# Kernel optimization log

Hardware: AMD Instinct MI355X
Metric: run time of the kernel (lower is better)

The kernel has to match this reference:

```python
import jax, jax.numpy as jnp
import numpy as np
from jax import lax

B, T, H, L = 64, 512, 768, 32
PAD = 0  # label_pad_token_id (NER_PAD_ID)


def setup_inputs() -> dict:
    key = jax.random.key(0)
    ks = jax.random.split(key, 8)
    hidden_states = jax.random.normal(ks[0], (B, T, H), jnp.float32)
    lengths = jax.random.randint(ks[1], (B,), T // 2, T + 1)
    attention_mask = (jnp.arange(T)[None, :] < lengths[:, None]).astype(jnp.int32)
    labels = jax.random.randint(ks[2], (B, T), 0, L).astype(jnp.int32)
    W = jax.random.normal(ks[3], (H, L), jnp.float32) * 0.02
    b = jnp.zeros((L,), jnp.float32)
    start_transitions = jax.random.uniform(ks[4], (L,), jnp.float32, -0.1, 0.1)
    end_transitions = jax.random.uniform(ks[5], (L,), jnp.float32, -0.1, 0.1)
    transitions = jax.random.uniform(ks[6], (L, L), jnp.float32, -0.1, 0.1)
    return dict(hidden_states=hidden_states, attention_mask=attention_mask,
                labels=labels, W=W, b=b, start_transitions=start_transitions,
                end_transitions=end_transitions, transitions=transitions)


def reference(hidden_states, attention_mask, labels, W, b,
              start_transitions, end_transitions, transitions):
    mask = attention_mask.astype(bool)          # [B,T], mask[:,0] all True
    mf = attention_mask.astype(hidden_states.dtype)
    # Dropout is identity at inference; emissions = Linear(hidden)
    emissions = hidden_states @ W + b            # [B,T,L]
    lengths = mask.sum(axis=1)                   # [B]

    # ---- CRF numerator (score of gold path) ----
    em_sc = jnp.take_along_axis(emissions, labels[..., None].astype(jnp.int32), axis=2)[..., 0]  # [B,T]
    tr_sc = transitions[labels[:, :-1], labels[:, 1:]]                                           # [B,T-1]
    last_tags = jnp.take_along_axis(labels, (lengths - 1)[:, None], axis=1)[:, 0]
    numer = (start_transitions[labels[:, 0]] + em_sc[:, 0]
             + jnp.sum((em_sc[:, 1:] + tr_sc) * mf[:, 1:], axis=1)
             + end_transitions[last_tags])

    # ---- CRF partition function (forward algorithm, scan over time) ----
    score0 = start_transitions + emissions[:, 0]                 # [B,L]
    em_rest = emissions[:, 1:].swapaxes(0, 1)                    # [T-1,B,L]
    m_rest = mask[:, 1:].T                                       # [T-1,B]

    def fstep(score, inp):
        em_t, m_t = inp
        nxt = jax.nn.logsumexp(score[:, :, None] + transitions[None], axis=1) + em_t
        return jnp.where(m_t[:, None], nxt, score), None

    scoreT, _ = lax.scan(fstep, score0, (em_rest, m_rest))
    denom = jax.nn.logsumexp(scoreT + end_transitions, axis=1)
    loss = -jnp.sum(numer - denom)               # torchcrf reduction='sum', times -1

    # ---- Viterbi decode ----
    def vstep(score, inp):
        em_t, m_t = inp
        x = score[:, :, None] + transitions[None]  # [B,L(prev),L(cur)]
        idx = jnp.argmax(x, axis=1)                # best prev tag per cur tag
        nxt = jnp.max(x, axis=1) + em_t
        return jnp.where(m_t[:, None], nxt, score), idx

    vT, hist = lax.scan(vstep, score0, (em_rest, m_rest))  # hist: [T-1,B,L]
    best_last = jnp.argmax(vT + end_transitions, axis=1).astype(jnp.int32)  # [B]
    last_idx = (lengths - 1).astype(jnp.int32)

    def bstep(carry, inp):
        h_t, t = inp                                            # h_t: [B,L]
        prev = jnp.take_along_axis(h_t, carry[:, None], axis=1)[:, 0].astype(jnp.int32)
        new_carry = jnp.where(t < last_idx, prev, best_last)
        out = jnp.where(t == last_idx, best_last,
                        jnp.where(t > last_idx, PAD, prev))
        return new_carry, out

    ts = jnp.arange(T - 2, -1, -1)
    _, outs = lax.scan(bstep, best_last, (hist[::-1], ts))      # outs: [T-1,B] for t=T-2..0
    tag_last = jnp.where(last_idx == T - 1, best_last, PAD)
    pred_labels = jnp.concatenate([jnp.flip(outs, 0), tag_last[None]], axis=0).T  # [B,T]
    return loss, pred_labels
```

## Files before the change

### kernel.cpp

```cpp
#include <hip/hip_runtime.h>

constexpr int Bn = 64, Tn = 512, Hn = 768, Ln = 32;

__global__ __launch_bounds__(256) void emis_gemm(const float* __restrict__ hs,
                                                 const float* __restrict__ W,
                                                 const float* __restrict__ bias,
                                                 float* __restrict__ em) {
  __shared__ __align__(16) float4 wl[Hn * 8];
  __shared__ __align__(16) float4 cbuf[128 * 8];
  const int tid = threadIdx.x;
  for (int it = tid; it < Hn * 8; it += 256) wl[it] = ((const float4*)W)[it];
  __syncthreads();
  const int half = tid >> 7;
  const int r = tid & 127;
  const long row = (long)blockIdx.x * 128 + r;
  const float* hb = hs + row * Hn + half * 384;
  const float4* wp = wl + half * 384 * 8;
  float4 acc[8];
#pragma unroll
  for (int c = 0; c < 8; ++c) acc[c] = make_float4(0.f, 0.f, 0.f, 0.f);
  for (int k4 = 0; k4 < 384; k4 += 4) {
    float4 h = *(const float4*)(hb + k4);
#pragma unroll
    for (int kk = 0; kk < 4; ++kk) {
      float hv = kk == 0 ? h.x : kk == 1 ? h.y : kk == 2 ? h.z : h.w;
      const float4* wr = wp + (k4 + kk) * 8;
#pragma unroll
      for (int c = 0; c < 8; ++c) {
        float4 wv = wr[c];
        acc[c].x = fmaf(hv, wv.x, acc[c].x);
        acc[c].y = fmaf(hv, wv.y, acc[c].y);
        acc[c].z = fmaf(hv, wv.z, acc[c].z);
        acc[c].w = fmaf(hv, wv.w, acc[c].w);
      }
    }
  }
  if (half == 1) {
#pragma unroll
    for (int c = 0; c < 8; ++c) cbuf[r * 8 + c] = acc[c];
  }
  __syncthreads();
  if (half == 0) {
#pragma unroll
    for (int c = 0; c < 8; ++c) {
      float4 p = cbuf[r * 8 + c];
      float4 bv = ((const float4*)bias)[c];
      float4 o = make_float4(acc[c].x + p.x + bv.x, acc[c].y + p.y + bv.y,
                             acc[c].z + p.z + bv.z, acc[c].w + p.w + bv.w);
      *(float4*)(em + row * Ln + c * 4) = o;
    }
  }
}

__global__ __launch_bounds__(512) void crf_scan(const float* __restrict__ em,
                                                const int* __restrict__ mask,
                                                const int* __restrict__ labels,
                                                const float* __restrict__ startT,
                                                const float* __restrict__ endT,
                                                const float* __restrict__ trans,
                                                float* __restrict__ outp) {
  __shared__ unsigned char hist[8][Tn][Ln];
  __shared__ __align__(16) float stage[8][64];
  __shared__ unsigned char Ctab[8][32][32];
  __shared__ int bnd[8][33];
  __shared__ int bl_lds[8];
  __shared__ int len_lds[8];

  const int tid = threadIdx.x;
  const int wid = tid >> 6;
  const int lane = tid & 63;
  const int half = lane >> 5;
  const int j = lane & 31;
  const bool is_vit = wid < 4;
  const int wb = ((wid & 3) << 1) + half;
  const int batch = blockIdx.x * 8 + wb;

  int s = 0;
  for (int t = j; t < Tn; t += 32) s += mask[batch * Tn + t];
#pragma unroll
  for (int m = 1; m <= 16; m <<= 1) s += __shfl_xor(s, m);
  const int len = s;
  const int lw = max(len, __shfl_xor(len, 32));
  const float* emb = em + (long)batch * Tn * Ln;

  if (is_vit) {
    if (j == 0) len_lds[wb] = len;
    float tr[32];
#pragma unroll
    for (int i = 0; i < 32; ++i) tr[i] = trans[i * Ln + j];
    float score = startT[j] + emb[j];
    float emn = emb[Ln + j];
    for (int t = 1; t < lw; ++t) {
      float em_t = emn;
      int tn = t + 1 < Tn ? t + 1 : Tn - 1;
      emn = emb[tn * Ln + j];
      stage[wid][lane] = score;
      const float* sb = &stage[wid][half * 32];
      float v[32];
#pragma unroll
      for (int q4 = 0; q4 < 8; ++q4) {
        float4 s4 = *(const float4*)(sb + q4 * 4);
        v[q4 * 4 + 0] = s4.x + tr[q4 * 4 + 0];
        v[q4 * 4 + 1] = s4.y + tr[q4 * 4 + 1];
        v[q4 * 4 + 2] = s4.z + tr[q4 * 4 + 2];
        v[q4 * 4 + 3] = s4.w + tr[q4 * 4 + 3];
      }
      float w[16];
#pragma unroll
      for (int q = 0; q < 16; ++q) w[q] = fmaxf(v[q], v[q + 16]);
#pragma unroll
      for (int sz = 8; sz >= 1; sz >>= 1)
#pragma unroll
        for (int q = 0; q < sz; ++q) w[q] = fmaxf(w[q], w[q + sz]);
      const float mv = w[0];
      int mi = 31;
#pragma unroll
      for (int i = 31; i >= 0; --i) mi = (v[i] == mv) ? i : mi;
      hist[wb][t - 1][j] = (unsigned char)mi;
      score = (t < len) ? (mv + em_t) : score;
    }
    for (int x = j; x < (Tn + 1 - len) * Ln; x += 32) {
      int rr = len - 1 + (x >> 5);
      hist[wb][rr][x & 31] = (unsigned char)(x & 31);
    }
    float bv = score + endT[j];
    int bj = j;
#pragma unroll
    for (int m = 1; m <= 16; m <<= 1) {
      float ov = __shfl_xor(bv, m);
      int oi = __shfl_xor(bj, m);
      if (ov > bv || (ov == bv && oi < bj)) { bv = ov; bj = oi; }
    }
    if (j == 0) bl_lds[wb] = bj;
  } else {
    float et[32];
#pragma unroll
    for (int i = 0; i < 32; ++i) et[i] = __expf(trans[i * Ln + j]);
    float score = startT[j] + emb[j];
    float emn = emb[Ln + j];
    for (int t = 1; t < lw; ++t) {
      float em_t = emn;
      int tn = t + 1 < Tn ? t + 1 : Tn - 1;
      emn = emb[tn * Ln + j];
      float s0 = __shfl(score, lane & 32);
      float e = __expf(score - s0);
      stage[wid][lane] = e;
      const float* eb = &stage[wid][half * 32];
      float a0 = 0.f, a1 = 0.f, a2 = 0.f, a3 = 0.f;
#pragma unroll
      for (int q = 0; q < 8; ++q) {
        float4 ev = *(const float4*)(eb + q * 4);
        a0 = fmaf(ev.x, et[q * 4 + 0], a0);
        a1 = fmaf(ev.y, et[q * 4 + 1], a1);
        a2 = fmaf(ev.z, et[q * 4 + 2], a2);
        a3 = fmaf(ev.w, et[q * 4 + 3], a3);
      }
      float nx = s0 + __logf((a0 + a1) + (a2 + a3)) + em_t;
      score = (t < len) ? nx : score;
    }
    float v = score + endT[j];
    float mx = v;
#pragma unroll
    for (int m = 1; m <= 16; m <<= 1) mx = fmaxf(mx, __shfl_xor(mx, m));
    float ssum = __expf(v - mx);
#pragma unroll
    for (int m = 1; m <= 16; m <<= 1) ssum += __shfl_xor(ssum, m);
    float denom = mx + __logf(ssum);
    float part = 0.f;
    const int* lab = labels + batch * Tn;
    for (int t = j; t < Tn; t += 32) {
      int lt = lab[t];
      if (t == 0)
        part += startT[lt] + emb[lt];
      else if (t < len)
        part += emb[t * Ln + lt] + trans[lab[t - 1] * Ln + lt];
    }
#pragma unroll
    for (int m = 1; m <= 16; m <<= 1) part += __shfl_xor(part, m);
    if (j == 0) {
      int lastl = lab[len - 1];
      atomicAdd(outp, denom - (part + endT[lastl]));
    }
  }
  __syncthreads();

  {
    const int wb2 = wid;
    const int batch2 = blockIdx.x * 8 + wb2;
    const int len2 = len_lds[wb2];
    const int best_last = bl_lds[wb2];
    const int kh2 = lane >> 5;
    int F[16];
#pragma unroll
    for (int kk = 0; kk < 16; ++kk) F[kk] = hist[wb2][16 * (kh2 * 16 + kk) + 15][j];
    for (int s2 = 14; s2 >= 0; --s2) {
#pragma unroll
      for (int kk = 0; kk < 16; ++kk) F[kk] = hist[wb2][16 * (kh2 * 16 + kk) + s2][F[kk]];
    }
#pragma unroll
    for (int kk = 0; kk < 16; ++kk) Ctab[wb2][kh2 * 16 + kk][j] = (unsigned char)F[kk];
    __syncthreads();
    if (lane == 0) {
      int c = best_last;
      bnd[wb2][32] = c;
      for (int k = 31; k >= 0; --k) {
        c = Ctab[wb2][k][c];
        bnd[wb2][k] = c;
      }
    }
    __syncthreads();
    if (lane < 32) {
      int c = bnd[wb2][lane + 1];
      float* po = outp + 1 + (long)batch2 * Tn;
#pragma unroll
      for (int s3 = 15; s3 >= 0; --s3) {
        int t = 16 * lane + s3;
        c = hist[wb2][t][c];
        po[t] = (t < len2) ? (float)c : 0.0f;
      }
    }
  }
}

extern "C" void kernel_launch(void* const* d_in, const int* in_sizes, int n_in,
                              void* d_out, int out_size, void* d_ws, size_t ws_size,
                              hipStream_t stream) {
  const float* hs = (const float*)d_in[0];
  const int* mask = (const int*)d_in[1];
  const int* labels = (const int*)d_in[2];
  const float* W = (const float*)d_in[3];
  const float* b = (const float*)d_in[4];
  const float* startT = (const float*)d_in[5];
  const float* endT = (const float*)d_in[6];
  const float* trans = (const float*)d_in[7];
  float* out = (float*)d_out;
  float* em = (float*)d_ws;

  emis_gemm<<<256, 256, 0, stream>>>(hs, W, b, em);
  hipMemsetAsync(d_out, 0, sizeof(float), stream);
  crf_scan<<<8, 512, 0, stream>>>(em, mask, labels, startT, endT, trans, out);
}
```

Measured before the change: 406.1 us.

## Spread CRF scan across more blocks and stage hidden rows via LDS in GEMM

The CRF scan now runs 32 blocks of 128 threads, each handling 2 batch rows, instead of 8 blocks of 512 threads handling 8 rows each. This spreads the serial time recurrence over more compute units and cuts per-block LDS. The emission GEMM stops staging all of W in LDS. It now loads coalesced 32-column chunks of hidden_states into a padded LDS tile with register prefetch and reads W straight from global or scalar memory using a wave-uniform index. The risk is more global or scalar load traffic for W in the inner loop, plus extra barriers per chunk.

```diff
diff --git a/kernel.cpp b/kernel.cpp
--- a/kernel.cpp
+++ b/kernel.cpp
@@ -6,74 +6,92 @@
                                                  const float* __restrict__ W,
                                                  const float* __restrict__ bias,
                                                  float* __restrict__ em) {
-  __shared__ __align__(16) float4 wl[Hn * 8];
-  __shared__ __align__(16) float4 cbuf[128 * 8];
+  __shared__ __align__(16) float tile[2][128][33];
   const int tid = threadIdx.x;
-  for (int it = tid; it < Hn * 8; it += 256) wl[it] = ((const float4*)W)[it];
+  const int hf = tid >> 7;
+  const int hfu = __builtin_amdgcn_readfirstlane(hf);
+  const int row = tid & 127;
+  const long row0 = (long)blockIdx.x * 128;
+
+  float4 ld[8];
+  int lc4[8], lr[8], lh2[8];
+#pragma unroll
+  for (int p = 0; p < 8; ++p) {
+    int fidx = p * 256 + tid;
+    lc4[p] = fidx & 7; lr[p] = (fidx >> 3) & 127; lh2[p] = fidx >> 10;
+  }
+
+  float acc[32];
+#pragma unroll
+  for (int c = 0; c < 32; ++c) acc[c] = 0.f;
+
+#pragma unroll
+  for (int p = 0; p < 8; ++p)
+    ld[p] = *(const float4*)(hs + (row0 + lr[p]) * Hn + lh2[p] * 384 + lc4[p] * 4);
+
+  for (int ch = 0; ch < 12; ++ch) {
+    __syncthreads();
+#pragma unroll
+    for (int p = 0; p < 8; ++p)
+      *(float4*)&tile[lh2[p]][lr[p]][lc4[p] * 4] = ld[p];
+    __syncthreads();
+    if (ch < 11) {
+#pragma unroll
+      for (int p = 0; p < 8; ++p)
+        ld[p] = *(const float4*)(hs + (row0 + lr[p]) * Hn + lh2[p] * 384 +
+                                 (ch + 1) * 32 + lc4[p] * 4);
+    }
+    const float* tp = &tile[hf][row][0];
+    const float* wb_ = W + (hfu * 384 + ch * 32) * Ln;
+#pragma unroll 4
+    for (int kk = 0; kk < 32; ++kk) {
+      float h = tp[kk];
+      const float* wr = wb_ + kk * Ln;
+#pragma unroll
+      for (int c = 0; c < 32; ++c) acc[c] = fmaf(h, wr[c], acc[c]);
+    }
+  }
   __syncthreads();
-  const int half = tid >> 7;
-  const int r = tid & 127;
-  const long row = (long)blockIdx.x * 128 + r;
-  const float* hb = hs + row * Hn + half * 384;
-  const float4* wp = wl + half * 384 * 8;
-  float4 acc[8];
-#pragma unroll
-  for (int c = 0; c < 8; ++c) acc[c] = make_float4(0.f, 0.f, 0.f, 0.f);
-  for (int k4 = 0; k4 < 384; k4 += 4) {
-    float4 h = *(const float4*)(hb + k4);
-#pragma unroll
-    for (int kk = 0; kk < 4; ++kk) {
-      float hv = kk == 0 ? h.x : kk == 1 ? h.y : kk == 2 ? h.z : h.w;
-      const float4* wr = wp + (k4 + kk) * 8;
-#pragma unroll
-      for (int c = 0; c < 8; ++c) {
-        float4 wv = wr[c];
-        acc[c].x = fmaf(hv, wv.x, acc[c].x);
-        acc[c].y = fmaf(hv, wv.y, acc[c].y);
-        acc[c].z = fmaf(hv, wv.z, acc[c].z);
-        acc[c].w = fmaf(hv, wv.w, acc[c].w);
-      }
-    }
-  }
-  if (half == 1) {
-#pragma unroll
-    for (int c = 0; c < 8; ++c) cbuf[r * 8 + c] = acc[c];
+  float* cb = &tile[0][0][0];
+  if (hf == 1) {
+#pragma unroll
+    for (int c = 0; c < 32; ++c) cb[row * 36 + c] = acc[c];
   }
   __syncthreads();
-  if (half == 0) {
-#pragma unroll
-    for (int c = 0; c < 8; ++c) {
-      float4 p = cbuf[r * 8 + c];
-      float4 bv = ((const float4*)bias)[c];
-      float4 o = make_float4(acc[c].x + p.x + bv.x, acc[c].y + p.y + bv.y,
-                             acc[c].z + p.z + bv.z, acc[c].w + p.w + bv.w);
-      *(float4*)(em + row * Ln + c * 4) = o;
+  if (hf == 0) {
+#pragma unroll
+    for (int c4 = 0; c4 < 8; ++c4) {
+      float4 p = *(float4*)&cb[row * 36 + c4 * 4];
+      float4 bv = ((const float4*)bias)[c4];
+      float4 o = make_float4((acc[c4 * 4 + 0] + p.x) + bv.x,
+                             (acc[c4 * 4 + 1] + p.y) + bv.y,
+                             (acc[c4 * 4 + 2] + p.z) + bv.z,
+                             (acc[c4 * 4 + 3] + p.w) + bv.w);
+      *(float4*)&em[(row0 + row) * Ln + c4 * 4] = o;
     }
   }
 }
 
-__global__ __launch_bounds__(512) void crf_scan(const float* __restrict__ em,
+__global__ __launch_bounds__(128) void crf_scan(const float* __restrict__ em,
                                                 const int* __restrict__ mask,
                                                 const int* __restrict__ labels,
                                                 const float* __restrict__ startT,
                                                 const float* __restrict__ endT,
                                                 const float* __restrict__ trans,
                                                 float* __restrict__ outp) {
-  __shared__ unsigned char hist[8][Tn][Ln];
-  __shared__ __align__(16) float stage[8][64];
-  __shared__ unsigned char Ctab[8][32][32];
-  __shared__ int bnd[8][33];
-  __shared__ int bl_lds[8];
-  __shared__ int len_lds[8];
+  __shared__ unsigned char hist[2][Tn][Ln];
+  __shared__ __align__(16) float stage[2][64];
+  __shared__ unsigned char Ctab[2][32][32];
+  __shared__ int bnd[2][33];
+  __shared__ int bl_lds[2];
+  __shared__ int len_lds[2];
 
   const int tid = threadIdx.x;
   const int wid = tid >> 6;
   const int lane = tid & 63;
   const int half = lane >> 5;
   const int j = lane & 31;
-  const bool is_vit = wid < 4;
-  const int wb = ((wid & 3) << 1) + half;
-  const int batch = blockIdx.x * 8 + wb;
+  const int batch = blockIdx.x * 2 + half;
 
   int s = 0;
   for (int t = j; t < Tn; t += 32) s += mask[batch * Tn + t];
@@ -83,8 +101,8 @@
   const int lw = max(len, __shfl_xor(len, 32));
   const float* emb = em + (long)batch * Tn * Ln;
 
-  if (is_vit) {
-    if (j == 0) len_lds[wb] = len;
+  if (wid == 0) {
+    if (j == 0) len_lds[half] = len;
     float tr[32];
 #pragma unroll
     for (int i = 0; i < 32; ++i) tr[i] = trans[i * Ln + j];
@@ -116,12 +134,12 @@
       int mi = 31;
 #pragma unroll
       for (int i = 31; i >= 0; --i) mi = (v[i] == mv) ? i : mi;
-      hist[wb][t - 1][j] = (unsigned char)mi;
+      hist[half][t - 1][j] = (unsigned char)mi;
       score = (t < len) ? (mv + em_t) : score;
     }
     for (int x = j; x < (Tn + 1 - len) * Ln; x += 32) {
       int rr = len - 1 + (x >> 5);
-      hist[wb][rr][x & 31] = (unsigned char)(x & 31);
+      hist[half][rr][x & 31] = (unsigned char)(x & 31);
     }
     float bv = score + endT[j];
     int bj = j;
@@ -131,7 +149,7 @@
       int oi = __shfl_xor(bj, m);
       if (ov > bv || (ov == bv && oi < bj)) { bv = ov; bj = oi; }
     }
-    if (j == 0) bl_lds[wb] = bj;
+    if (j == 0) bl_lds[half] = bj;
   } else {
     float et[32];
 #pragma unroll
@@ -186,7 +204,7 @@
 
   {
     const int wb2 = wid;
-    const int batch2 = blockIdx.x * 8 + wb2;
+    const int batch2 = blockIdx.x * 2 + wb2;
     const int len2 = len_lds[wb2];
     const int best_last = bl_lds[wb2];
     const int kh2 = lane >> 5;
@@ -238,5 +256,5 @@
 
   emis_gemm<<<256, 256, 0, stream>>>(hs, W, b, em);
   hipMemsetAsync(d_out, 0, sizeof(float), stream);
-  crf_scan<<<8, 512, 0, stream>>>(em, mask, labels, startT, endT, trans, out);
+  crf_scan<<<32, 128, 0, stream>>>(em, mask, labels, startT, endT, trans, out);
 }
```

New measurement: 471.9 us. 1.16x slower.
